# Kernel tuning notes

Measured on AMD Instinct MI355X. Metric: run time of the kernel, lower is better.

## Reference

```python
import jax, jax.numpy as jnp
import numpy as np

K = 64        # num_clusters
S1 = 5        # num_shadow + 1
C = 128       # dim
ALPHA = 1500.0
EPS = 1e-12


def setup_inputs() -> dict:
    key = jax.random.key(0)
    k1, k2 = jax.random.split(key)
    x = jax.random.normal(k1, (8, C, 44, 44), dtype=jnp.float32)
    centroids = jax.random.normal(k2, (K, S1, C), dtype=jnp.float32) * 0.01
    return {"x": x, "centroids": centroids}


def reference(x, centroids):
    N = x.shape[0]
    # conv params derived from centroids, as in _init_params
    w = (2.0 * ALPHA) * centroids.reshape(K * S1, C)            # (K*S1, C)
    b = -ALPHA * jnp.linalg.norm(centroids.reshape(K * S1, C), axis=1)  # (K*S1,)

    xf = x.reshape(N, C, -1)                                    # (N, C, P)
    # 1x1 conv == GEMM over channel dim
    logits = jnp.einsum('mc,ncp->nmp', w, xf) + b[None, :, None]
    logits = logits.reshape(N, K, S1, -1)                       # (N, K, S1, P)

    soft_alpha = jax.nn.softmax(logits[:, :, 0:1, :], axis=1)   # (N, K, 1, P)
    soft_beta = jax.nn.softmax(logits, axis=2)[:, :, 0:1, :]    # (N, K, 1, P)
    soft_assign = soft_alpha * soft_beta                        # (N, K, 1, P)

    # residual = x - rep_centroid; then residual *= (1 + soft_assign); sum over P.
    # sum_p (x[n,c,p] - rep[k,c]) * w[n,k,p]
    #   = einsum(w, x) - rep[k,c] * sum_p w[n,k,p]   (same math, no (N,K,C,P) tensor)
    w_assign = 1.0 + soft_assign[:, :, 0, :]                    # (N, K, P)
    rep = centroids[:, 0, :]                                    # (K, C)
    out = jnp.einsum('nkp,ncp->nkc', w_assign, xf) \
          - rep[None, :, :] * jnp.sum(w_assign, axis=-1)[:, :, None]  # (N, K, C)

    # intra-cluster L2 normalize (dim=2), flatten, global L2 normalize
    out = out / jnp.maximum(jnp.linalg.norm(out, axis=2, keepdims=True), EPS)
    flat = out.reshape(N, -1)
    flat = flat / jnp.maximum(jnp.linalg.norm(flat, axis=1, keepdims=True), EPS)
    return (flat, soft_assign)
```

## Files before the change

kernel.cpp:

```cpp
#include <hip/hip_runtime.h>
#include <math.h>

#define NB 8
#define KC 64
#define S1C 5
#define CC 128
#define PP 1936
#define MM 320
#define PT 64
#define NPT 31
#define NTILE (NB * NPT)
#define ALPHAF 1500.0f
#define EPSF 1e-12f

#define WS_CENPK 65536
#define WS_GBIAS 512
#define WS_HDR   (WS_CENPK + WS_GBIAS)
#define WS_PART  ((size_t)NTILE * KC * CC)
#define WS_MAIN_FLOATS (WS_HDR + WS_PART + (size_t)NTILE * KC)

typedef __attribute__((ext_vector_type(8))) short short8;
typedef __attribute__((ext_vector_type(4))) float f32x4;

__device__ __forceinline__ unsigned pack_bf16s(float x) {
    unsigned u  = __float_as_uint(x);
    unsigned hi = u & 0xffff0000u;
    float lo    = x - __uint_as_float(hi);
    return hi | (__float_as_uint(lo) >> 16);
}

__device__ __forceinline__ void unpack8(const int4 q0, const int4 q1,
                                        short8& h, short8& l) {
    const int d[8] = {q0.x, q0.y, q0.z, q0.w, q1.x, q1.y, q1.z, q1.w};
#pragma unroll
    for (int j = 0; j < 8; ++j) {
        h[j] = (short)((unsigned)d[j] >> 16);
        l[j] = (short)((unsigned)d[j] & 0xffffu);
    }
}

__device__ __forceinline__ void split8(const float4 a, const float4 b,
                                       short8& h, short8& l) {
    const float f[8] = {a.x, a.y, a.z, a.w, b.x, b.y, b.z, b.w};
#pragma unroll
    for (int j = 0; j < 8; ++j) {
        const unsigned u  = __float_as_uint(f[j]);
        const unsigned hi = u & 0xffff0000u;
        const float lo    = f[j] - __uint_as_float(hi);
        h[j] = (short)(hi >> 16);
        l[j] = (short)(__float_as_uint(lo) >> 16);
    }
}

__global__ __launch_bounds__(64) void k0_pack(
    const float* __restrict__ cen, unsigned* __restrict__ cenPk,
    float* __restrict__ gbias)
{
    const int nt   = blockIdx.x;
    const int l    = threadIdx.x;
    const int l15  = l & 15;
    const int quad = l >> 4;
    const int mp   = nt * 16 + l15;
    const int s    = mp & 7;
    const bool valid = (s < 5);
    const int wrow = 5 * (mp >> 3) + s;
    short8* dst8 = (short8*)cenPk;
    float ss = 0.f;
#pragma unroll
    for (int ks = 0; ks < 4; ++ks) {
        float4 v0 = make_float4(0.f, 0.f, 0.f, 0.f), v1 = v0;
        if (valid) {
            const float* wp = cen + (size_t)wrow * CC + ks * 32 + quad * 8;
            v0 = *(const float4*)wp;
            v1 = *(const float4*)(wp + 4);
        }
        ss += v0.x * v0.x + v0.y * v0.y + v0.z * v0.z + v0.w * v0.w
            + v1.x * v1.x + v1.y * v1.y + v1.z * v1.z + v1.w * v1.w;
        short8 h, lo;
        split8(v0, v1, h, lo);
        const int base = ((ks * 32 + nt) * 64 + l) * 2;
        dst8[base]     = h;
        dst8[base + 1] = lo;
    }
    ss += __shfl_xor(ss, 16);
    ss += __shfl_xor(ss, 32);
    if (quad == 0) gbias[mp] = valid ? (-ALPHAF * sqrtf(ss)) : -3.0e38f;
}

__global__ __launch_bounds__(1024, 4) void k1_main(
    const float* __restrict__ x, const unsigned* __restrict__ cenPk,
    const float* __restrict__ gbias,
    float* __restrict__ sa_out, float* __restrict__ outC,
    float* __restrict__ outS, int mode)
{
    __shared__ unsigned xbuf[CC * 68];
    __shared__ unsigned war[KC * 68];
    __shared__ float2   ap[16 * 66];

    const int tid  = threadIdx.x;
    const int lane = tid & 63;
    const int wid  = tid >> 6;
    const int quad = lane >> 4;
    const int l15  = lane & 15;
    const int bx   = blockIdx.x;
    const int n    = bx / NPT;
    const int pt   = bx - n * NPT;
    const int p0   = pt * PT;

    const float bv0 = gbias[(2 * wid + 0) * 16 + l15];
    const float bv1 = gbias[(2 * wid + 1) * 16 + l15];
    const short8* cpk8 = (const short8*)cenPk;
    short8 bh0[2], bl0[2];
#pragma unroll
    for (int i = 0; i < 2; ++i) {
        const int boff = ((2 * wid + i) * 64 + lane) * 2;
        bh0[i] = cpk8[boff];
        bl0[i] = cpk8[boff + 1];
    }

    const float* xn = x + (size_t)n * CC * PP;
    const int sc  = tid >> 3;
    const int spo = (tid & 7) * 8;
    unsigned pk[8];
    {
        float4 v0 = make_float4(0.f, 0.f, 0.f, 0.f), v1 = v0;
        if (p0 + spo < PP) {
            const float* src = xn + (size_t)sc * PP + p0 + spo;
            v0 = *(const float4*)src;
            v1 = *(const float4*)(src + 4);
        }
        pk[0] = pack_bf16s(v0.x); pk[1] = pack_bf16s(v0.y);
        pk[2] = pack_bf16s(v0.z); pk[3] = pack_bf16s(v0.w);
        pk[4] = pack_bf16s(v1.x); pk[5] = pack_bf16s(v1.y);
        pk[6] = pack_bf16s(v1.z); pk[7] = pack_bf16s(v1.w);
#pragma unroll
        for (int j = 0; j < 8; ++j) xbuf[(spo + j) * 132 + sc] = pk[j];
    }
    __syncthreads();

    f32x4 dacc[4][2];
#pragma unroll
    for (int a = 0; a < 4; ++a) {
        dacc[a][0] = (f32x4){0.f, 0.f, 0.f, 0.f};
        dacc[a][1] = (f32x4){0.f, 0.f, 0.f, 0.f};
    }

    auto mfma_step = [&](const int ksoff, const short8 bh[2], const short8 bl[2]) {
#pragma unroll
        for (int a = 0; a < 4; ++a) {
            const int abase = (a * 16 + l15) * 132 + ksoff + quad * 8;
            const int4 q0 = *(const int4*)(&xbuf[abase]);
            const int4 q1 = *(const int4*)(&xbuf[abase + 4]);
            short8 ah, al;
            unpack8(q0, q1, ah, al);
#pragma unroll
            for (int i = 0; i < 2; ++i) {
                dacc[a][i] = __builtin_amdgcn_mfma_f32_16x16x32_bf16(ah, bh[i], dacc[a][i], 0, 0, 0);
                dacc[a][i] = __builtin_amdgcn_mfma_f32_16x16x32_bf16(ah, bl[i], dacc[a][i], 0, 0, 0);
                dacc[a][i] = __builtin_amdgcn_mfma_f32_16x16x32_bf16(al, bh[i], dacc[a][i], 0, 0, 0);
            }
        }
    };

    mfma_step(0, bh0, bl0);
#pragma unroll 1
    for (int ks = 1; ks < 4; ++ks) {
        short8 bh[2], bl[2];
#pragma unroll
        for (int i = 0; i < 2; ++i) {
            const int boff = ((ks * 32 + 2 * wid + i) * 64 + lane) * 2;
            bh[i] = cpk8[boff];
            bl[i] = cpk8[boff + 1];
        }
        mfma_step(ks * 32, bh, bl);
    }

#pragma unroll
    for (int a = 0; a < 4; ++a)
#pragma unroll
        for (int r = 0; r < 4; ++r) {
            dacc[a][0][r] = 2.f * ALPHAF * dacc[a][0][r] + bv0;
            dacc[a][1][r] = 2.f * ALPHAF * dacc[a][1][r] + bv1;
        }

#pragma unroll
    for (int a = 0; a < 4; ++a) {
        f32x4 mx4, se4;
#pragma unroll
        for (int r = 0; r < 4; ++r) {
            float m_ = fmaxf(dacc[a][0][r], dacc[a][1][r]);
            m_ = fmaxf(m_, __shfl_xor(m_, 8));
            float se = __expf(dacc[a][0][r] - m_) + __expf(dacc[a][1][r] - m_);
            se += __shfl_xor(se, 8);
            mx4[r] = m_; se4[r] = se;
        }
        if (l15 == 0) {
#pragma unroll
            for (int r = 0; r < 4; ++r)
                ap[wid * 66 + a * 16 + 4 * quad + r] = make_float2(mx4[r], se4[r]);
        }
    }
    __syncthreads();

    *(int4*)(&xbuf[sc * 68 + spo])     = *(const int4*)&pk[0];
    *(int4*)(&xbuf[sc * 68 + spo + 4]) = *(const int4*)&pk[4];

    float gmv, arv;
    {
        float gm = -3.0e38f;
#pragma unroll
        for (int w = 0; w < 16; ++w) gm = fmaxf(gm, ap[w * 66 + lane].x);
        float s = 0.f;
#pragma unroll
        for (int w = 0; w < 16; ++w) {
            const float2 v = ap[w * 66 + lane];
            s += v.y * __expf(v.x - gm);
        }
        gmv = gm; arv = 1.0f / s;
    }

    float psum[2] = {0.f, 0.f};
    const bool is_s0 = ((l15 & 7) == 0);
#pragma unroll
    for (int a = 0; a < 4; ++a) {
#pragma unroll
        for (int i = 0; i < 2; ++i) {
            const f32x4 lg = dacc[a][i];
            unsigned wpk[4];
#pragma unroll
            for (int r = 0; r < 4; ++r) {
                float m_ = lg[r];
                m_ = fmaxf(m_, __shfl_xor(m_, 1));
                m_ = fmaxf(m_, __shfl_xor(m_, 2));
                m_ = fmaxf(m_, __shfl_xor(m_, 4));
                const float e_ = __expf(lg[r] - m_);
                float d_ = e_;
                d_ += __shfl_xor(d_, 1);
                d_ += __shfl_xor(d_, 2);
                d_ += __shfl_xor(d_, 4);
                const int p = a * 16 + 4 * quad + r;
                const float gm_p = __shfl(gmv, p);
                const float ar_p = __shfl(arv, p);
                const float sa = __expf(lg[r] - gm_p) * ar_p * (e_ / d_);
                const bool pvalid = (p0 + p) < PP;
                const float wa = pvalid ? (1.0f + sa) : 0.0f;
                wpk[r] = pack_bf16s(wa);
                psum[i] += wa;
            }
            const int k = 4 * wid + 2 * i + (l15 >> 3);
            if (is_s0)
                *(int4*)(&war[k * 68 + a * 16 + 4 * quad]) = *(const int4*)wpk;
        }
    }
#pragma unroll
    for (int i = 0; i < 2; ++i) {
        float s = psum[i];
        s += __shfl_xor(s, 16);
        s += __shfl_xor(s, 32);
        if (is_s0 && quad == 0) {
            const int k = 4 * wid + 2 * i + (l15 >> 3);
            if (mode == 0) outS[(size_t)bx * KC + k] = s;
            else           atomicAdd(&outS[(size_t)n * KC + k], s);
        }
    }
    __syncthreads();

    const int kt  = wid & 3;
    const int ct0 = (wid >> 2) * 2;
    f32x4 cacc[2];
    cacc[0] = (f32x4){0.f, 0.f, 0.f, 0.f};
    cacc[1] = (f32x4){0.f, 0.f, 0.f, 0.f};
#pragma unroll
    for (int ks = 0; ks < 64; ks += 32) {
        const int abase = (kt * 16 + l15) * 68 + ks + quad * 8;
        const int4 qa0 = *(const int4*)(&war[abase]);
        const int4 qa1 = *(const int4*)(&war[abase + 4]);
        short8 ah, al;
        unpack8(qa0, qa1, ah, al);
#pragma unroll
        for (int t = 0; t < 2; ++t) {
            const int c = (ct0 + t) * 16 + l15;
            const int bbase = c * 68 + ks + quad * 8;
            const int4 qb0 = *(const int4*)(&xbuf[bbase]);
            const int4 qb1 = *(const int4*)(&xbuf[bbase + 4]);
            short8 bh, bl;
            unpack8(qb0, qb1, bh, bl);
            cacc[t] = __builtin_amdgcn_mfma_f32_16x16x32_bf16(ah, bh, cacc[t], 0, 0, 0);
            cacc[t] = __builtin_amdgcn_mfma_f32_16x16x32_bf16(ah, bl, cacc[t], 0, 0, 0);
            cacc[t] = __builtin_amdgcn_mfma_f32_16x16x32_bf16(al, bh, cacc[t], 0, 0, 0);
        }
    }
    if (mode == 0) {
        float* dst = outC + (size_t)bx * KC * CC;
#pragma unroll
        for (int t = 0; t < 2; ++t) {
            const int c = (ct0 + t) * 16 + l15;
#pragma unroll
            for (int r = 0; r < 4; ++r)
                dst[(kt * 16 + 4 * quad + r) * CC + c] = cacc[t][r];
        }
    } else {
        float* dst = outC + (size_t)n * KC * CC;
#pragma unroll
        for (int t = 0; t < 2; ++t) {
            const int c = (ct0 + t) * 16 + l15;
#pragma unroll
            for (int r = 0; r < 4; ++r)
                atomicAdd(&dst[(kt * 16 + 4 * quad + r) * CC + c], cacc[t][r]);
        }
    }

    {
        float* san = sa_out + (size_t)n * KC * PP;
        const int k  = tid >> 4;
        const int p4 = (tid & 15) * 4;
        const int pg = p0 + p4;
        if (pg < PP) {
            const int4 q = *(const int4*)(&war[k * 68 + p4]);
            const int d[4] = {q.x, q.y, q.z, q.w};
            float4 sv;
            float* svp = &sv.x;
#pragma unroll
            for (int j = 0; j < 4; ++j) {
                const unsigned u = (unsigned)d[j];
                const float wa = __uint_as_float(u & 0xffff0000u)
                               + __uint_as_float(u << 16);
                svp[j] = wa - 1.0f;
            }
            *(float4*)(&san[(size_t)k * PP + pg]) = sv;
        }
    }
}

__global__ __launch_bounds__(128) void k2_slab(
    const float* __restrict__ part, const float* __restrict__ ps,
    const float* __restrict__ cen, float* __restrict__ flat)
{
    __shared__ float w2[2];
    const int b = blockIdx.x;
    const int n = b >> 6;
    const int k = b & 63;
    const int c = threadIdx.x;
    const float* pb = part + (size_t)n * NPT * KC * CC + (size_t)k * CC + c;
    float v = 0.f;
#pragma unroll 8
    for (int pt = 0; pt < NPT; ++pt) v += pb[(size_t)pt * KC * CC];
    const float* psb = ps + (size_t)n * NPT * KC + k;
    float sw = 0.f;
#pragma unroll
    for (int pt = 0; pt < NPT; ++pt) sw += psb[(size_t)pt * KC];
    v -= cen[(size_t)k * S1C * CC + c] * sw;

    float ss = v * v;
#pragma unroll
    for (int off = 32; off > 0; off >>= 1) ss += __shfl_down(ss, off);
    if ((c & 63) == 0) w2[c >> 6] = ss;
    __syncthreads();
    const float norm = sqrtf(w2[0] + w2[1]);
    const float scale = 1.0f / (fmaxf(norm, EPSF) * 8.0f);
    flat[(size_t)b * CC + c] = v * scale;
}

__global__ __launch_bounds__(128) void k2_final(
    const float* __restrict__ accC, const float* __restrict__ accS,
    const float* __restrict__ cen, float* __restrict__ flat)
{
    __shared__ float w2[2];
    const int b = blockIdx.x;
    const int k = b & 63;
    const int c = threadIdx.x;
    const float v = accC[(size_t)b * CC + c] -
                    cen[(size_t)k * S1C * CC + c] * accS[b];
    float ss = v * v;
#pragma unroll
    for (int off = 32; off > 0; off >>= 1) ss += __shfl_down(ss, off);
    if ((c & 63) == 0) w2[c >> 6] = ss;
    __syncthreads();
    const float norm = sqrtf(w2[0] + w2[1]);
    const float scale = 1.0f / (fmaxf(norm, EPSF) * 8.0f);
    flat[(size_t)b * CC + c] = v * scale;
}

extern "C" void kernel_launch(void* const* d_in, const int* in_sizes, int n_in,
                              void* d_out, int out_size, void* d_ws, size_t ws_size,
                              hipStream_t stream) {
    const float* x   = (const float*)d_in[0];
    const float* cen = (const float*)d_in[1];
    float* out  = (float*)d_out;
    float* flat = out;
    float* sa   = out + (size_t)NB * KC * CC;
    float* ws   = (float*)d_ws;

    unsigned* cenPk = (unsigned*)ws;
    float*    gbias = ws + WS_CENPK;

    if (ws_size >= WS_MAIN_FLOATS * 4) {
        float* part = ws + WS_HDR;
        float* ps   = part + WS_PART;
        k0_pack<<<32, 64, 0, stream>>>(cen, cenPk, gbias);
        k1_main<<<NTILE, 1024, 0, stream>>>(x, cenPk, gbias, sa, part, ps, 0);
        k2_slab<<<NB * KC, 128, 0, stream>>>(part, ps, cen, flat);
    } else {
        float* accC = ws + WS_HDR;
        float* accS = accC + (size_t)NB * KC * CC;
        hipMemsetAsync(accC, 0, (size_t)(NB * KC * CC + NB * KC) * 4, stream);
        k0_pack<<<32, 64, 0, stream>>>(cen, cenPk, gbias);
        k1_main<<<NTILE, 1024, 0, stream>>>(x, cenPk, gbias, sa, accC, accS, 1);
        k2_final<<<NB * KC, 128, 0, stream>>>(accC, accS, cen, flat);
    }
}
```

Baseline: 91.14 us.

## Transpose first MFMA so shadow logits sit in per-lane registers, cutting softmax shuffles

Swaps the MFMA operand order in the logits GEMM so each lane's accumulator holds the shadow-dimension logits for one pixel rather than four pixels. The per-cluster softmax over S1 then needs only one cross-lane shuffle instead of three-step butterfly reductions for max and sum. The bias is loaded as a float4 to match the new layout. The stats, weight write and row-sum reductions are rewritten to follow the new lane mapping, which risks indexing mistakes in the packed layout.

```diff
diff --git a/kernel.cpp b/kernel.cpp
--- a/kernel.cpp
+++ b/kernel.cpp
@@ -107,15 +107,17 @@
     const int pt   = bx - n * NPT;
     const int p0   = pt * PT;
 
-    const float bv0 = gbias[(2 * wid + 0) * 16 + l15];
-    const float bv1 = gbias[(2 * wid + 1) * 16 + l15];
+    float4 bvf[2];
+#pragma unroll
+    for (int i = 0; i < 2; ++i)
+        bvf[i] = *(const float4*)(gbias + (2 * wid + i) * 16 + quad * 4);
     const short8* cpk8 = (const short8*)cenPk;
-    short8 bh0[2], bl0[2];
+    short8 ch0[2], cl0[2];
 #pragma unroll
     for (int i = 0; i < 2; ++i) {
         const int boff = ((2 * wid + i) * 64 + lane) * 2;
-        bh0[i] = cpk8[boff];
-        bl0[i] = cpk8[boff + 1];
+        ch0[i] = cpk8[boff];
+        cl0[i] = cpk8[boff + 1];
     }
 
     const float* xn = x + (size_t)n * CC * PP;
@@ -145,60 +147,56 @@
         dacc[a][1] = (f32x4){0.f, 0.f, 0.f, 0.f};
     }
 
-    auto mfma_step = [&](const int ksoff, const short8 bh[2], const short8 bl[2]) {
+    auto mfma_step = [&](const int ksoff, const short8 ch[2], const short8 cl[2]) {
 #pragma unroll
         for (int a = 0; a < 4; ++a) {
             const int abase = (a * 16 + l15) * 132 + ksoff + quad * 8;
             const int4 q0 = *(const int4*)(&xbuf[abase]);
             const int4 q1 = *(const int4*)(&xbuf[abase + 4]);
-            short8 ah, al;
-            unpack8(q0, q1, ah, al);
+            short8 xh, xl;
+            unpack8(q0, q1, xh, xl);
 #pragma unroll
             for (int i = 0; i < 2; ++i) {
-                dacc[a][i] = __builtin_amdgcn_mfma_f32_16x16x32_bf16(ah, bh[i], dacc[a][i], 0, 0, 0);
-                dacc[a][i] = __builtin_amdgcn_mfma_f32_16x16x32_bf16(ah, bl[i], dacc[a][i], 0, 0, 0);
-                dacc[a][i] = __builtin_amdgcn_mfma_f32_16x16x32_bf16(al, bh[i], dacc[a][i], 0, 0, 0);
+                dacc[a][i] = __builtin_amdgcn_mfma_f32_16x16x32_bf16(ch[i], xh, dacc[a][i], 0, 0, 0);
+                dacc[a][i] = __builtin_amdgcn_mfma_f32_16x16x32_bf16(ch[i], xl, dacc[a][i], 0, 0, 0);
+                dacc[a][i] = __builtin_amdgcn_mfma_f32_16x16x32_bf16(cl[i], xh, dacc[a][i], 0, 0, 0);
             }
         }
     };
 
-    mfma_step(0, bh0, bl0);
+    mfma_step(0, ch0, cl0);
 #pragma unroll 1
     for (int ks = 1; ks < 4; ++ks) {
-        short8 bh[2], bl[2];
+        short8 ch[2], cl[2];
 #pragma unroll
         for (int i = 0; i < 2; ++i) {
             const int boff = ((ks * 32 + 2 * wid + i) * 64 + lane) * 2;
-            bh[i] = cpk8[boff];
-            bl[i] = cpk8[boff + 1];
-        }
-        mfma_step(ks * 32, bh, bl);
-    }
-
-#pragma unroll
-    for (int a = 0; a < 4; ++a)
-#pragma unroll
-        for (int r = 0; r < 4; ++r) {
-            dacc[a][0][r] = 2.f * ALPHAF * dacc[a][0][r] + bv0;
-            dacc[a][1][r] = 2.f * ALPHAF * dacc[a][1][r] + bv1;
-        }
+            ch[i] = cpk8[boff];
+            cl[i] = cpk8[boff + 1];
+        }
+        mfma_step(ks * 32, ch, cl);
+    }
+
+#pragma unroll
+    for (int i = 0; i < 2; ++i) {
+        const float* bvp = (const float*)&bvf[i];
+#pragma unroll
+        for (int a = 0; a < 4; ++a)
+#pragma unroll
+            for (int r = 0; r < 4; ++r)
+                dacc[a][i][r] = 2.f * ALPHAF * dacc[a][i][r] + bvp[r];
+    }
 
 #pragma unroll
     for (int a = 0; a < 4; ++a) {
-        f32x4 mx4, se4;
-#pragma unroll
-        for (int r = 0; r < 4; ++r) {
-            float m_ = fmaxf(dacc[a][0][r], dacc[a][1][r]);
-            m_ = fmaxf(m_, __shfl_xor(m_, 8));
-            float se = __expf(dacc[a][0][r] - m_) + __expf(dacc[a][1][r] - m_);
-            se += __shfl_xor(se, 8);
-            mx4[r] = m_; se4[r] = se;
-        }
-        if (l15 == 0) {
-#pragma unroll
-            for (int r = 0; r < 4; ++r)
-                ap[wid * 66 + a * 16 + 4 * quad + r] = make_float2(mx4[r], se4[r]);
-        }
+        const float l0 = dacc[a][0][0];
+        const float l1 = dacc[a][1][0];
+        const float m2 = fmaxf(l0, l1);
+        const float mo = __shfl_xor(m2, 32);
+        const float m4 = fmaxf(m2, mo);
+        float se = __expf(l0 - m4) + __expf(l1 - m4);
+        se += __shfl_xor(se, 32);
+        if ((lane & 48) == 0) ap[wid * 66 + a * 16 + l15] = make_float2(m4, se);
     }
     __syncthreads();
 
@@ -219,46 +217,39 @@
         gmv = gm; arv = 1.0f / s;
     }
 
-    float psum[2] = {0.f, 0.f};
-    const bool is_s0 = ((l15 & 7) == 0);
+    const int  kb  = 4 * wid + ((lane >> 5) & 1);
+    const bool evq = ((lane & 16) == 0);
+    float psum2[2] = {0.f, 0.f};
 #pragma unroll
     for (int a = 0; a < 4; ++a) {
+        const int p = a * 16 + l15;
+        const float gm_p = __shfl(gmv, p);
+        const float ar_p = __shfl(arv, p);
+        const bool pvalid = (p0 + p) < PP;
 #pragma unroll
         for (int i = 0; i < 2; ++i) {
             const f32x4 lg = dacc[a][i];
-            unsigned wpk[4];
-#pragma unroll
-            for (int r = 0; r < 4; ++r) {
-                float m_ = lg[r];
-                m_ = fmaxf(m_, __shfl_xor(m_, 1));
-                m_ = fmaxf(m_, __shfl_xor(m_, 2));
-                m_ = fmaxf(m_, __shfl_xor(m_, 4));
-                const float e_ = __expf(lg[r] - m_);
-                float d_ = e_;
-                d_ += __shfl_xor(d_, 1);
-                d_ += __shfl_xor(d_, 2);
-                d_ += __shfl_xor(d_, 4);
-                const int p = a * 16 + 4 * quad + r;
-                const float gm_p = __shfl(gmv, p);
-                const float ar_p = __shfl(arv, p);
-                const float sa = __expf(lg[r] - gm_p) * ar_p * (e_ / d_);
-                const bool pvalid = (p0 + p) < PP;
-                const float wa = pvalid ? (1.0f + sa) : 0.0f;
-                wpk[r] = pack_bf16s(wa);
-                psum[i] += wa;
-            }
-            const int k = 4 * wid + 2 * i + (l15 >> 3);
-            if (is_s0)
-                *(int4*)(&war[k * 68 + a * 16 + 4 * quad]) = *(const int4*)wpk;
+            const float s4 = __shfl_xor(lg[0], 16);
+            float m5 = fmaxf(fmaxf(lg[0], lg[1]), fmaxf(lg[2], lg[3]));
+            m5 = fmaxf(m5, s4);
+            const float e0 = __expf(lg[0] - m5);
+            const float d5 = e0 + __expf(lg[1] - m5) + __expf(lg[2] - m5)
+                           + __expf(lg[3] - m5) + __expf(s4 - m5);
+            const float sa = __expf(lg[0] - gm_p) * ar_p * (e0 / d5);
+            const float wa = pvalid ? (1.0f + sa) : 0.0f;
+            if (evq) war[(kb + 2 * i) * 68 + p] = pack_bf16s(wa);
+            psum2[i] += wa;
         }
     }
 #pragma unroll
     for (int i = 0; i < 2; ++i) {
-        float s = psum[i];
-        s += __shfl_xor(s, 16);
-        s += __shfl_xor(s, 32);
-        if (is_s0 && quad == 0) {
-            const int k = 4 * wid + 2 * i + (l15 >> 3);
+        float s = psum2[i];
+        s += __shfl_xor(s, 1);
+        s += __shfl_xor(s, 2);
+        s += __shfl_xor(s, 4);
+        s += __shfl_xor(s, 8);
+        if ((lane & 31) == 0) {
+            const int k = kb + 2 * i;
             if (mode == 0) outS[(size_t)bx * KC + k] = s;
             else           atomicAdd(&outS[(size_t)n * KC + k], s);
         }
```

Result: faster. 80.62 us (-11.5%).
